# Performance work log

Hardware: AMD Instinct MI355X
Metric: run time of the kernel (lower is better)

## Reference

```python
import jax, jax.numpy as jnp
import numpy as np

EMB = 512
LIN = 64
ATT = 64
H = 8
EPS = 1e-6


def layer_norm(x, eps=EPS):
    # layer norm over last dim, no affine params (matches F.layer_norm w/o weight/bias)
    mu = jnp.mean(x, axis=-1, keepdims=True)
    var = jnp.var(x, axis=-1, keepdims=True)
    return (x - mu) * jax.lax.rsqrt(var + eps)


def setup_inputs() -> dict:
    key = jax.random.key(0)
    k1, k2, k3, k4, k5 = jax.random.split(key, 5)
    B, N = 8, 2048
    x = jax.random.normal(k1, (B, N, EMB), dtype=jnp.float32)
    rel_pos_bias = jax.random.normal(k2, (H, N, N), dtype=jnp.float32)
    invalid_attn_mask = jnp.ones((B, N, N), dtype=jnp.float32)
    uvqk = jax.random.normal(k3, (EMB, LIN * 2 * H + ATT * H * 2), dtype=jnp.float32) * 0.02
    o_w = jax.random.normal(k4, (EMB, LIN * H), dtype=jnp.float32) * (1.0 / np.sqrt(LIN * H))
    o_b = jnp.zeros((EMB,), dtype=jnp.float32)
    return {"x": x, "rel_pos_bias": rel_pos_bias, "invalid_attn_mask": invalid_attn_mask,
            "uvqk": uvqk, "o_w": o_w, "o_b": o_b}


def reference(x, rel_pos_bias, invalid_attn_mask, uvqk, o_w, o_b):
    B, N, D = x.shape
    residual = x
    normed = layer_norm(x)                                   # [B,N,D]
    proj = jax.nn.silu(jnp.einsum('bnd,de->bne', normed, uvqk))  # [B,N,2*LIN*H+2*ATT*H]
    lh = LIN * H
    ah = ATT * H
    u = proj[..., :lh]                                        # [B,N,LIN*H]
    v = proj[..., lh:2 * lh].reshape(B, N, H, LIN)            # [B,N,H,LIN]
    q = proj[..., 2 * lh:2 * lh + ah].reshape(B, N, H, ATT)
    k = proj[..., 2 * lh + ah:].reshape(B, N, H, ATT)
    qk = jnp.einsum('bnhd,bmhd->bhnm', q, k) + rel_pos_bias[None]  # [B,H,N,N]
    qk = jax.nn.silu(qk) * invalid_attn_mask[:, None]
    attn = jnp.einsum('bhnm,bmhd->bnhd', qk, v).reshape(B, N, lh)
    gated = u * layer_norm(attn)
    out = jnp.einsum('bnf,ef->bne', gated, o_w) + o_b          # dropout off (eval)
    return residual + out
```

## Files before the change

kernel.cpp:

```cpp
#include <hip/hip_runtime.h>
#include <stdint.h>

typedef short bf16x8   __attribute__((ext_vector_type(8)));
typedef short short4v  __attribute__((ext_vector_type(4)));
typedef short short8v  __attribute__((ext_vector_type(8)));
typedef float f32x4    __attribute__((ext_vector_type(4)));

typedef __attribute__((address_space(3))) uint32_t lds_u32;
typedef const __attribute__((address_space(1))) uint32_t glob_u32;

__device__ __forceinline__ void gl_lds16(const void* g, void* l) {
  __builtin_amdgcn_global_load_lds((glob_u32*)g, (lds_u32*)l, 16, 0, 0);
}

__device__ __forceinline__ float bf2f(short u) {
  union { float f; uint32_t i; } v; v.i = ((uint32_t)(uint16_t)u) << 16; return v.f;
}
__device__ __forceinline__ short f2bf(float f) {
  union { float f; uint32_t i; } v; v.f = f;
  uint32_t r = v.i + 0x7FFFu + ((v.i >> 16) & 1u);
  return (short)(r >> 16);
}
__device__ __forceinline__ float siluf(float x) {
  return x * __builtin_amdgcn_rcpf(1.0f + __expf(-x));
}
__device__ __forceinline__ f32x4 mfma16(bf16x8 a, bf16x8 b, f32x4 c) {
  return __builtin_amdgcn_mfma_f32_16x16x32_bf16(a, b, c, 0, 0, 0);
}

__global__ __launch_bounds__(256) void k_ln(const float* __restrict__ x, short* __restrict__ xn) {
  int row = blockIdx.x * 4 + (threadIdx.x >> 6);
  int lane = threadIdx.x & 63;
  const float4* xr = (const float4*)(x + (size_t)row * 512);
  float4 a = xr[lane * 2], b = xr[lane * 2 + 1];
  float s  = a.x + a.y + a.z + a.w + b.x + b.y + b.z + b.w;
  float s2 = a.x*a.x + a.y*a.y + a.z*a.z + a.w*a.w + b.x*b.x + b.y*b.y + b.z*b.z + b.w*b.w;
#pragma unroll
  for (int m = 1; m < 64; m <<= 1) { s += __shfl_xor(s, m); s2 += __shfl_xor(s2, m); }
  float mu = s * (1.f / 512.f);
  float rstd = rsqrtf(s2 * (1.f / 512.f) - mu * mu + 1e-6f);
  float v[8] = {a.x, a.y, a.z, a.w, b.x, b.y, b.z, b.w};
  short8v o;
#pragma unroll
  for (int j = 0; j < 8; ++j) o[j] = f2bf((v[j] - mu) * rstd);
  *(short8v*)&xn[(size_t)row * 512 + lane * 8] = o;
}

__global__ __launch_bounds__(256) void k_prep_w(const float* __restrict__ uvqk, short* __restrict__ Wt) {
  __shared__ float t[64][65];
  int k0 = blockIdx.x * 64;
  int c0 = blockIdx.y * 64;
  for (int i = threadIdx.x; i < 64 * 64; i += 256) {
    int r = i >> 6, c = i & 63;
    t[r][c] = uvqk[(size_t)(k0 + r) * 2048 + c0 + c];
  }
  __syncthreads();
  for (int i = threadIdx.x; i < 64 * 64; i += 256) {
    int c = i >> 6, k = i & 63;
    Wt[(size_t)(c0 + c) * 512 + k0 + k] = f2bf(t[k][c]);
  }
}

__global__ __launch_bounds__(256) void k_cast_ow(const float* __restrict__ ow, short* __restrict__ owt) {
  int i = blockIdx.x * 256 + threadIdx.x;
  owt[i] = f2bf(ow[i]);
}

__device__ __forceinline__ void gemm_core(const short* __restrict__ A, const short* __restrict__ Bt,
                                          int t0, int c0, short* As, short* Bs, f32x4 (&acc)[4][4]) {
  int tid = threadIdx.x;
  int w = tid >> 6, lane = tid & 63, l16 = lane & 15, lq = lane >> 4;
  int wm = (w >> 1) * 64, wn = (w & 1) * 64;
  int srow = tid >> 3;
  int sch = (tid & 7) ^ (srow & 7);
  const short* ag = A  + (size_t)(t0 + srow) * 512 + sch * 8;
  const short* bg = Bt + (size_t)(c0 + srow) * 512 + sch * 8;

  for (int k0 = 0; k0 < 512; k0 += 64) {
#pragma unroll
    for (int j = 0; j < 4; ++j) {
      gl_lds16(ag + (size_t)j * 32 * 512 + k0, (char*)As + j * 4096 + w * 1024);
      gl_lds16(bg + (size_t)j * 32 * 512 + k0, (char*)Bs + j * 4096 + w * 1024);
    }
    asm volatile("s_waitcnt vmcnt(0)" ::: "memory");
    __syncthreads();
#pragma unroll
    for (int kk = 0; kk < 2; ++kk) {
      bf16x8 af[4], bf[4];
#pragma unroll
      for (int mi = 0; mi < 4; ++mi) {
        int row = wm + mi * 16 + l16;
        af[mi] = *(const bf16x8*)&As[row * 64 + (((kk * 4 + lq) ^ (l16 & 7)) * 8)];
      }
#pragma unroll
      for (int ni = 0; ni < 4; ++ni) {
        int row = wn + ni * 16 + l16;
        bf[ni] = *(const bf16x8*)&Bs[row * 64 + (((kk * 4 + lq) ^ (l16 & 7)) * 8)];
      }
#pragma unroll
      for (int mi = 0; mi < 4; ++mi)
#pragma unroll
        for (int ni = 0; ni < 4; ++ni)
          acc[mi][ni] = mfma16(af[mi], bf[ni], acc[mi][ni]);
    }
    __syncthreads();
  }
}

__global__ __launch_bounds__(256) void k_gemm1(const short* __restrict__ A, const short* __restrict__ Bt,
                                               short* __restrict__ proj, short* __restrict__ Vt) {
  __shared__ short As[128 * 64], Bs[128 * 64];
  int c0 = blockIdx.x * 128, t0 = blockIdx.y * 128;
  f32x4 acc[4][4] = {};
  gemm_core(A, Bt, t0, c0, As, Bs, acc);
  int tid = threadIdx.x, w = tid >> 6, lane = tid & 63, l16 = lane & 15, lq = lane >> 4;
  int wm = (w >> 1) * 64, wn = (w & 1) * 64;
  bool isv = (c0 >= 512 && c0 < 1024);
#pragma unroll
  for (int mi = 0; mi < 4; ++mi)
#pragma unroll
    for (int ni = 0; ni < 4; ++ni) {
      int c = c0 + wn + ni * 16 + l16;
      int trow = t0 + wm + mi * 16 + lq * 4;
      if (isv) {
        int hh = (c - 512) >> 6, d = (c - 512) & 63;
        int bb = trow >> 11, nn = trow & 2047;
        short4v pv;
#pragma unroll
        for (int i = 0; i < 4; ++i) pv[i] = f2bf(siluf(acc[mi][ni][i]));
        *(short4v*)&Vt[((size_t)(bb * 8 + hh) * 64 + d) * 2048 + nn] = pv;
      } else {
#pragma unroll
        for (int i = 0; i < 4; ++i)
          proj[(size_t)(trow + i) * 2048 + c] = f2bf(siluf(acc[mi][ni][i]));
      }
    }
}

__global__ __launch_bounds__(256, 3) void k_attn(const short* __restrict__ proj,
                                                 const short* __restrict__ Vt,
                                                 const float* __restrict__ rpb,
                                                 const float* __restrict__ maskp,
                                                 float* __restrict__ attn) {
  __shared__ __align__(16) short Ks[2][64 * 64];
  __shared__ __align__(16) short Vs[2][64 * 64];
  __shared__ __align__(16) short Ps[128 * 64];

  int p = blockIdx.x;
  int L = (p & 7) * 128 + (p >> 3);
  int qt = L >> 6, h = (L >> 3) & 7, b = L & 7;
  int n0 = qt * 128;

  int tid = threadIdx.x;
  int w = tid >> 6, lane = tid & 63, l16 = lane & 15, lq = lane >> 4;

  bf16x8 qf[2][2];
#pragma unroll
  for (int mi = 0; mi < 2; ++mi)
#pragma unroll
    for (int kk = 0; kk < 2; ++kk) {
      int n = n0 + w * 32 + mi * 16 + l16;
      qf[mi][kk] = *(const bf16x8*)&proj[(size_t)(b * 2048 + n) * 2048 + 1024 + h * 64 + kk * 32 + lq * 8];
    }

  int j8 = lane >> 3, c8 = lane & 7;
  int srcc = (c8 ^ j8) * 8;
  const short* kg = proj + (size_t)(b * 2048) * 2048 + 1536 + h * 64 + srcc;
  const short* vg = Vt + (size_t)((b * 8 + h) * 64) * 2048 + srcc;

  const float* rp_t = rpb   + (size_t)h * 4194304 + (size_t)(n0 + w * 32 + l16) * 2048 + lq * 4;
  const float* mk_t = maskp + (size_t)b * 4194304 + (size_t)(n0 + w * 32 + l16) * 2048 + lq * 4;

  f32x4 acc_o[2][4] = {};

#pragma unroll
  for (int j = 0; j < 2; ++j) {
    gl_lds16(kg + (size_t)(w * 16 + j * 8 + j8) * 2048, &Ks[0][w * 1024 + j * 512]);
    gl_lds16(vg + (size_t)(w * 16 + j * 8 + j8) * 2048, &Vs[0][w * 1024 + j * 512]);
  }
  asm volatile("s_waitcnt vmcnt(0)" ::: "memory");
  __builtin_amdgcn_s_barrier();

  for (int t = 0; t < 32; ++t) {
    int kv0 = t << 6;
    const short* Kc = Ks[t & 1];
    const short* Vc = Vs[t & 1];

    if (t < 31) {
      short* Kn = Ks[(t & 1) ^ 1];
      short* Vn = Vs[(t & 1) ^ 1];
      int kvn = kv0 + 64;
#pragma unroll
      for (int j = 0; j < 2; ++j) {
        gl_lds16(kg + (size_t)(kvn + w * 16 + j * 8 + j8) * 2048, &Kn[w * 1024 + j * 512]);
        gl_lds16(vg + (size_t)(w * 16 + j * 8 + j8) * 2048 + kvn, &Vn[w * 1024 + j * 512]);
      }
    }

    f32x4 rv0[4], mv0[4];
#pragma unroll
    for (int ni = 0; ni < 4; ++ni) {
      rv0[ni] = *(const f32x4*)(rp_t + kv0 + ni * 16);
      mv0[ni] = *(const f32x4*)(mk_t + kv0 + ni * 16);
    }

    f32x4 s[4][2];
#pragma unroll
    for (int ni = 0; ni < 4; ++ni)
#pragma unroll
      for (int mi = 0; mi < 2; ++mi) s[ni][mi] = (f32x4){0.f, 0.f, 0.f, 0.f};
    __builtin_amdgcn_s_setprio(1);
#pragma unroll
    for (int kk = 0; kk < 2; ++kk) {
      bf16x8 kf[4];
#pragma unroll
      for (int ni = 0; ni < 4; ++ni)
        kf[ni] = *(const bf16x8*)&Kc[(ni * 16 + l16) * 64 + (((kk * 4 + lq) ^ (l16 & 7)) * 8)];
#pragma unroll
      for (int ni = 0; ni < 4; ++ni)
#pragma unroll
        for (int mi = 0; mi < 2; ++mi)
          s[ni][mi] = mfma16(kf[ni], qf[mi][kk], s[ni][mi]);
    }
    __builtin_amdgcn_s_setprio(0);

    f32x4 rv1[4], mv1[4];
#pragma unroll
    for (int ni = 0; ni < 4; ++ni) {
      rv1[ni] = *(const f32x4*)(rp_t + 16 * 2048 + kv0 + ni * 16);
      mv1[ni] = *(const f32x4*)(mk_t + 16 * 2048 + kv0 + ni * 16);
    }

    {
      int row = w * 32 + l16;
      char* pr = (char*)Ps + row * 128;
      int swz = (l16 & 7) << 4;
#pragma unroll
      for (int ni = 0; ni < 4; ++ni) {
        short4v pk;
#pragma unroll
        for (int i = 0; i < 4; ++i) {
          float xx = s[ni][0][i] + rv0[ni][i];
          pk[i] = f2bf(siluf(xx) * mv0[ni][i]);
        }
        *(short4v*)(pr + ((ni * 32 + lq * 8) ^ swz)) = pk;
      }
    }
    {
      int row = w * 32 + 16 + l16;
      char* pr = (char*)Ps + row * 128;
      int swz = (l16 & 7) << 4;
#pragma unroll
      for (int ni = 0; ni < 4; ++ni) {
        short4v pk;
#pragma unroll
        for (int i = 0; i < 4; ++i) {
          float xx = s[ni][1][i] + rv1[ni][i];
          pk[i] = f2bf(siluf(xx) * mv1[ni][i]);
        }
        *(short4v*)(pr + ((ni * 32 + lq * 8) ^ swz)) = pk;
      }
    }

    __builtin_amdgcn_s_setprio(1);
#pragma unroll
    for (int ks = 0; ks < 2; ++ks) {
      bf16x8 pf[2], vf[4];
#pragma unroll
      for (int mi = 0; mi < 2; ++mi) {
        int rp = w * 32 + mi * 16 + l16;
        pf[mi] = *(const bf16x8*)((const char*)Ps + rp * 128 + (((ks * 4 + lq) << 4) ^ ((l16 & 7) << 4)));
      }
#pragma unroll
      for (int ni = 0; ni < 4; ++ni)
        vf[ni] = *(const bf16x8*)&Vc[(ni * 16 + l16) * 64 + (((ks * 4 + lq) ^ (l16 & 7)) * 8)];
#pragma unroll
      for (int mi = 0; mi < 2; ++mi)
#pragma unroll
        for (int ni = 0; ni < 4; ++ni)
          acc_o[mi][ni] = mfma16(pf[mi], vf[ni], acc_o[mi][ni]);
    }
    __builtin_amdgcn_s_setprio(0);

    asm volatile("s_waitcnt vmcnt(0)" ::: "memory");
    __builtin_amdgcn_s_barrier();
  }

#pragma unroll
  for (int mi = 0; mi < 2; ++mi)
#pragma unroll
    for (int ni = 0; ni < 4; ++ni)
#pragma unroll
      for (int i = 0; i < 4; ++i) {
        int n = n0 + w * 32 + mi * 16 + lq * 4 + i;
        attn[(size_t)(b * 2048 + n) * 512 + h * 64 + ni * 16 + l16] = acc_o[mi][ni][i];
      }
}

__global__ __launch_bounds__(256) void k_gate(const float* __restrict__ attn, const short* __restrict__ proj,
                                              short* __restrict__ gated) {
  int row = blockIdx.x * 4 + (threadIdx.x >> 6);
  int lane = threadIdx.x & 63;
  const float4* ar = (const float4*)(attn + (size_t)row * 512);
  float4 a = ar[lane * 2], b = ar[lane * 2 + 1];
  float s  = a.x + a.y + a.z + a.w + b.x + b.y + b.z + b.w;
  float s2 = a.x*a.x + a.y*a.y + a.z*a.z + a.w*a.w + b.x*b.x + b.y*b.y + b.z*b.z + b.w*b.w;
#pragma unroll
  for (int m = 1; m < 64; m <<= 1) { s += __shfl_xor(s, m); s2 += __shfl_xor(s2, m); }
  float mu = s * (1.f / 512.f);
  float rstd = rsqrtf(s2 * (1.f / 512.f) - mu * mu + 1e-6f);
  float v[8] = {a.x, a.y, a.z, a.w, b.x, b.y, b.z, b.w};
  short8v u = *(const short8v*)&proj[(size_t)row * 2048 + lane * 8];
  short8v g;
#pragma unroll
  for (int j = 0; j < 8; ++j) g[j] = f2bf(bf2f(u[j]) * ((v[j] - mu) * rstd));
  *(short8v*)&gated[(size_t)row * 512 + lane * 8] = g;
}

__global__ __launch_bounds__(256) void k_gemm2(const short* __restrict__ A, const short* __restrict__ Bt,
                                               const float* __restrict__ ob, const float* __restrict__ x,
                                               float* __restrict__ out) {
  __shared__ short As[128 * 64], Bs[128 * 64];
  int c0 = blockIdx.x * 128, t0 = blockIdx.y * 128;
  f32x4 acc[4][4] = {};
  gemm_core(A, Bt, t0, c0, As, Bs, acc);
  int tid = threadIdx.x, w = tid >> 6, lane = tid & 63, l16 = lane & 15, lq = lane >> 4;
  int wm = (w >> 1) * 64, wn = (w & 1) * 64;
#pragma unroll
  for (int mi = 0; mi < 4; ++mi)
#pragma unroll
    for (int ni = 0; ni < 4; ++ni) {
      int e = c0 + wn + ni * 16 + l16;
      float bias = ob[e];
#pragma unroll
      for (int i = 0; i < 4; ++i) {
        int t = t0 + wm + mi * 16 + lq * 4 + i;
        out[(size_t)t * 512 + e] = acc[mi][ni][i] + bias + x[(size_t)t * 512 + e];
      }
    }
}

extern "C" void kernel_launch(void* const* d_in, const int* in_sizes, int n_in,
                              void* d_out, int out_size, void* d_ws, size_t ws_size,
                              hipStream_t stream) {
  const float* x    = (const float*)d_in[0];
  const float* rpb  = (const float*)d_in[1];
  const float* mask = (const float*)d_in[2];
  const float* uvqk = (const float*)d_in[3];
  const float* o_w  = (const float*)d_in[4];
  const float* o_b  = (const float*)d_in[5];
  float* out = (float*)d_out;

  char* p = (char*)d_ws;
  short* xn   = (short*)p; p += 16384ull * 512 * 2;
  short* Wt   = (short*)p; p += 2048ull * 512 * 2;
  short* owt  = (short*)p; p += 512ull * 512 * 2;
  short* proj = (short*)p; p += 16384ull * 2048 * 2;
  short* Vt   = (short*)p; p += 8ull * 8 * 64 * 2048 * 2;
  float* attn = (float*)p; p += 16384ull * 512 * 4;
  short* gated = xn;

  k_ln    <<<4096, 256, 0, stream>>>(x, xn);
  k_prep_w<<<dim3(8, 32), 256, 0, stream>>>(uvqk, Wt);
  k_cast_ow<<<1024, 256, 0, stream>>>(o_w, owt);
  k_gemm1 <<<dim3(16, 128), 256, 0, stream>>>(xn, Wt, proj, Vt);
  k_attn  <<<1024, 256, 0, stream>>>(proj, Vt, rpb, mask, attn);
  k_gate  <<<4096, 256, 0, stream>>>(attn, proj, gated);
  k_gemm2 <<<dim3(4, 128), 256, 0, stream>>>(gated, owt, o_b, x, out);
}
```

Before: 392.3 us.

## Cast bias and mask to bf16 and prefetch them one tile ahead

Adds a vectorised cast kernel that converts the relative position bias and the attention mask to bf16 in workspace on every call. The attention kernel is templated so it reads these half-width copies when the workspace is large enough. It also loads the bias and mask values for the next KV tile at the end of each iteration, waiting with a partial vmcnt instead of a full drain. This roughly halves the bias and mask traffic that each attention block re-reads across heads and batches, at the price of an extra full pass over both fp32 tensors and bf16 rounding of the bias.

```diff
diff --git a/kernel.cpp b/kernel.cpp
--- a/kernel.cpp
+++ b/kernel.cpp
@@ -64,6 +64,18 @@
 __global__ __launch_bounds__(256) void k_cast_ow(const float* __restrict__ ow, short* __restrict__ owt) {
   int i = blockIdx.x * 256 + threadIdx.x;
   owt[i] = f2bf(ow[i]);
+}
+
+__global__ __launch_bounds__(256) void k_cast_bf(const float* __restrict__ src, short* __restrict__ dst, int n8) {
+  for (int i = blockIdx.x * 256 + threadIdx.x; i < n8; i += gridDim.x * 256) {
+    const float4* s4 = (const float4*)src + (size_t)i * 2;
+    float4 a = s4[0], b = s4[1];
+    float v[8] = {a.x, a.y, a.z, a.w, b.x, b.y, b.z, b.w};
+    short8v o;
+#pragma unroll
+    for (int j = 0; j < 8; ++j) o[j] = f2bf(v[j]);
+    *(short8v*)&dst[(size_t)i * 8] = o;
+  }
 }
 
 __device__ __forceinline__ void gemm_core(const short* __restrict__ A, const short* __restrict__ Bt,
@@ -137,10 +149,11 @@
     }
 }
 
+template<bool BF>
 __global__ __launch_bounds__(256, 3) void k_attn(const short* __restrict__ proj,
                                                  const short* __restrict__ Vt,
-                                                 const float* __restrict__ rpb,
-                                                 const float* __restrict__ maskp,
+                                                 const void* __restrict__ rpbp,
+                                                 const void* __restrict__ maskp,
                                                  float* __restrict__ attn) {
   __shared__ __align__(16) short Ks[2][64 * 64];
   __shared__ __align__(16) short Vs[2][64 * 64];
@@ -168,17 +181,36 @@
   const short* kg = proj + (size_t)(b * 2048) * 2048 + 1536 + h * 64 + srcc;
   const short* vg = Vt + (size_t)((b * 8 + h) * 64) * 2048 + srcc;
 
-  const float* rp_t = rpb   + (size_t)h * 4194304 + (size_t)(n0 + w * 32 + l16) * 2048 + lq * 4;
-  const float* mk_t = maskp + (size_t)b * 4194304 + (size_t)(n0 + w * 32 + l16) * 2048 + lq * 4;
+  size_t rbase = (size_t)h * 4194304 + (size_t)(n0 + w * 32 + l16) * 2048 + lq * 4;
+  size_t mbase = (size_t)b * 4194304 + (size_t)(n0 + w * 32 + l16) * 2048 + lq * 4;
 
   f32x4 acc_o[2][4] = {};
+
+  short4v rvb[2][4], mvb[2][4];
+  f32x4   rvf[2][4], mvf[2][4];
 
 #pragma unroll
   for (int j = 0; j < 2; ++j) {
     gl_lds16(kg + (size_t)(w * 16 + j * 8 + j8) * 2048, &Ks[0][w * 1024 + j * 512]);
     gl_lds16(vg + (size_t)(w * 16 + j * 8 + j8) * 2048, &Vs[0][w * 1024 + j * 512]);
   }
-  asm volatile("s_waitcnt vmcnt(0)" ::: "memory");
+  __builtin_amdgcn_sched_barrier(0);
+#pragma unroll
+  for (int mi = 0; mi < 2; ++mi)
+#pragma unroll
+    for (int ni = 0; ni < 4; ++ni) {
+      size_t off = (size_t)mi * 16 * 2048 + ni * 16;
+      if constexpr (BF) {
+        rvb[mi][ni] = *(const short4v*)((const short*)rpbp + rbase + off);
+        mvb[mi][ni] = *(const short4v*)((const short*)maskp + mbase + off);
+      } else {
+        rvf[mi][ni] = *(const f32x4*)((const float*)rpbp + rbase + off);
+        mvf[mi][ni] = *(const f32x4*)((const float*)maskp + mbase + off);
+      }
+    }
+  __builtin_amdgcn_sched_barrier(0);
+  asm volatile("s_waitcnt vmcnt(16)" ::: "memory");
+  __builtin_amdgcn_sched_barrier(0);
   __builtin_amdgcn_s_barrier();
 
   for (int t = 0; t < 32; ++t) {
@@ -196,13 +228,7 @@
         gl_lds16(vg + (size_t)(w * 16 + j * 8 + j8) * 2048 + kvn, &Vn[w * 1024 + j * 512]);
       }
     }
-
-    f32x4 rv0[4], mv0[4];
-#pragma unroll
-    for (int ni = 0; ni < 4; ++ni) {
-      rv0[ni] = *(const f32x4*)(rp_t + kv0 + ni * 16);
-      mv0[ni] = *(const f32x4*)(mk_t + kv0 + ni * 16);
-    }
+    __builtin_amdgcn_sched_barrier(0);
 
     f32x4 s[4][2];
 #pragma unroll
@@ -224,15 +250,9 @@
     }
     __builtin_amdgcn_s_setprio(0);
 
-    f32x4 rv1[4], mv1[4];
-#pragma unroll
-    for (int ni = 0; ni < 4; ++ni) {
-      rv1[ni] = *(const f32x4*)(rp_t + 16 * 2048 + kv0 + ni * 16);
-      mv1[ni] = *(const f32x4*)(mk_t + 16 * 2048 + kv0 + ni * 16);
-    }
-
-    {
-      int row = w * 32 + l16;
+#pragma unroll
+    for (int mi = 0; mi < 2; ++mi) {
+      int row = w * 32 + mi * 16 + l16;
       char* pr = (char*)Ps + row * 128;
       int swz = (l16 & 7) << 4;
 #pragma unroll
@@ -240,23 +260,11 @@
         short4v pk;
 #pragma unroll
         for (int i = 0; i < 4; ++i) {
-          float xx = s[ni][0][i] + rv0[ni][i];
-          pk[i] = f2bf(siluf(xx) * mv0[ni][i]);
-        }
-        *(short4v*)(pr + ((ni * 32 + lq * 8) ^ swz)) = pk;
-      }
-    }
-    {
-      int row = w * 32 + 16 + l16;
-      char* pr = (char*)Ps + row * 128;
-      int swz = (l16 & 7) << 4;
-#pragma unroll
-      for (int ni = 0; ni < 4; ++ni) {
-        short4v pk;
-#pragma unroll
-        for (int i = 0; i < 4; ++i) {
-          float xx = s[ni][1][i] + rv1[ni][i];
-          pk[i] = f2bf(siluf(xx) * mv1[ni][i]);
+          float r, m;
+          if constexpr (BF) { r = bf2f(rvb[mi][ni][i]); m = bf2f(mvb[mi][ni][i]); }
+          else              { r = rvf[mi][ni][i];       m = mvf[mi][ni][i]; }
+          float xx = s[ni][mi][i] + r;
+          pk[i] = f2bf(siluf(xx) * m);
         }
         *(short4v*)(pr + ((ni * 32 + lq * 8) ^ swz)) = pk;
       }
@@ -282,7 +290,26 @@
     }
     __builtin_amdgcn_s_setprio(0);
 
-    asm volatile("s_waitcnt vmcnt(0)" ::: "memory");
+    __builtin_amdgcn_sched_barrier(0);
+    {
+      int kvp = (t < 31) ? kv0 + 64 : kv0;
+#pragma unroll
+      for (int mi = 0; mi < 2; ++mi)
+#pragma unroll
+        for (int ni = 0; ni < 4; ++ni) {
+          size_t off = (size_t)mi * 16 * 2048 + kvp + ni * 16;
+          if constexpr (BF) {
+            rvb[mi][ni] = *(const short4v*)((const short*)rpbp + rbase + off);
+            mvb[mi][ni] = *(const short4v*)((const short*)maskp + mbase + off);
+          } else {
+            rvf[mi][ni] = *(const f32x4*)((const float*)rpbp + rbase + off);
+            mvf[mi][ni] = *(const f32x4*)((const float*)maskp + mbase + off);
+          }
+        }
+    }
+    __builtin_amdgcn_sched_barrier(0);
+    asm volatile("s_waitcnt vmcnt(16)" ::: "memory");
+    __builtin_amdgcn_sched_barrier(0);
     __builtin_amdgcn_s_barrier();
   }
 
@@ -358,13 +385,24 @@
   short* proj = (short*)p; p += 16384ull * 2048 * 2;
   short* Vt   = (short*)p; p += 8ull * 8 * 64 * 2048 * 2;
   float* attn = (float*)p; p += 16384ull * 512 * 4;
+  short* rpbh = (short*)p; p += 33554432ull * 2;
+  short* mskh = (short*)p; p += 33554432ull * 2;
   short* gated = xn;
+
+  bool bf_ok = ws_size >= (size_t)((char*)p - (char*)d_ws);
 
   k_ln    <<<4096, 256, 0, stream>>>(x, xn);
   k_prep_w<<<dim3(8, 32), 256, 0, stream>>>(uvqk, Wt);
   k_cast_ow<<<1024, 256, 0, stream>>>(o_w, owt);
+  if (bf_ok) {
+    k_cast_bf<<<4096, 256, 0, stream>>>(rpb,  rpbh, 33554432 / 8);
+    k_cast_bf<<<4096, 256, 0, stream>>>(mask, mskh, 33554432 / 8);
+  }
   k_gemm1 <<<dim3(16, 128), 256, 0, stream>>>(xn, Wt, proj, Vt);
-  k_attn  <<<1024, 256, 0, stream>>>(proj, Vt, rpb, mask, attn);
+  if (bf_ok)
+    k_attn<true> <<<1024, 256, 0, stream>>>(proj, Vt, rpbh, mskh, attn);
+  else
+    k_attn<false><<<1024, 256, 0, stream>>>(proj, Vt, rpb, mask, attn);
   k_gate  <<<4096, 256, 0, stream>>>(attn, proj, gated);
   k_gemm2 <<<dim3(4, 128), 256, 0, stream>>>(gated, owt, o_b, x, out);
 }
```

Measured after the change: 477.6 us. 21.8% more time.

## Halve attention query tile, prefetch bias/mask one step ahead, use packed bf16 convert

Applied to the files above, without the earlier changes.

The attention kernel now handles 64 query rows per block instead of 128 and launches twice as many blocks. It also declares 4 waves per SIMD in launch bounds instead of 3 and halves the P scratch buffer. The rel_pos_bias and mask loads for the next KV tile are issued at the end of each iteration, with a partial vmcnt wait, so the dominant fp32 bias and mask streams overlap compute. The P tile is converted with v_cvt_pk_bf16_f32 instead of manual rounding. Smaller tiles double K/V reloads from L2 in exchange for higher occupancy and latency hiding.

```diff
diff --git a/kernel.cpp b/kernel.cpp
--- a/kernel.cpp
+++ b/kernel.cpp
@@ -26,6 +26,11 @@
 }
 __device__ __forceinline__ f32x4 mfma16(bf16x8 a, bf16x8 b, f32x4 c) {
   return __builtin_amdgcn_mfma_f32_16x16x32_bf16(a, b, c, 0, 0, 0);
+}
+__device__ __forceinline__ uint32_t cvtpk_bf16(float lo, float hi) {
+  uint32_t d;
+  asm("v_cvt_pk_bf16_f32 %0, %1, %2" : "=v"(d) : "v"(lo), "v"(hi));
+  return d;
 }
 
 __global__ __launch_bounds__(256) void k_ln(const float* __restrict__ x, short* __restrict__ xn) {
@@ -137,48 +142,55 @@
     }
 }
 
-__global__ __launch_bounds__(256, 3) void k_attn(const short* __restrict__ proj,
+__global__ __launch_bounds__(256, 4) void k_attn(const short* __restrict__ proj,
                                                  const short* __restrict__ Vt,
                                                  const float* __restrict__ rpb,
                                                  const float* __restrict__ maskp,
                                                  float* __restrict__ attn) {
   __shared__ __align__(16) short Ks[2][64 * 64];
   __shared__ __align__(16) short Vs[2][64 * 64];
-  __shared__ __align__(16) short Ps[128 * 64];
+  __shared__ __align__(16) short Ps[64 * 64];
 
   int p = blockIdx.x;
-  int L = (p & 7) * 128 + (p >> 3);
+  int L = (p & 7) * 256 + (p >> 3);
   int qt = L >> 6, h = (L >> 3) & 7, b = L & 7;
-  int n0 = qt * 128;
+  int n0 = qt * 64;
 
   int tid = threadIdx.x;
   int w = tid >> 6, lane = tid & 63, l16 = lane & 15, lq = lane >> 4;
 
-  bf16x8 qf[2][2];
-#pragma unroll
-  for (int mi = 0; mi < 2; ++mi)
-#pragma unroll
-    for (int kk = 0; kk < 2; ++kk) {
-      int n = n0 + w * 32 + mi * 16 + l16;
-      qf[mi][kk] = *(const bf16x8*)&proj[(size_t)(b * 2048 + n) * 2048 + 1024 + h * 64 + kk * 32 + lq * 8];
-    }
+  bf16x8 qf[2];
+#pragma unroll
+  for (int kk = 0; kk < 2; ++kk) {
+    int n = n0 + w * 16 + l16;
+    qf[kk] = *(const bf16x8*)&proj[(size_t)(b * 2048 + n) * 2048 + 1024 + h * 64 + kk * 32 + lq * 8];
+  }
 
   int j8 = lane >> 3, c8 = lane & 7;
   int srcc = (c8 ^ j8) * 8;
   const short* kg = proj + (size_t)(b * 2048) * 2048 + 1536 + h * 64 + srcc;
   const short* vg = Vt + (size_t)((b * 8 + h) * 64) * 2048 + srcc;
 
-  const float* rp_t = rpb   + (size_t)h * 4194304 + (size_t)(n0 + w * 32 + l16) * 2048 + lq * 4;
-  const float* mk_t = maskp + (size_t)b * 4194304 + (size_t)(n0 + w * 32 + l16) * 2048 + lq * 4;
-
-  f32x4 acc_o[2][4] = {};
+  const float* rp_t = rpb   + (size_t)h * 4194304 + (size_t)(n0 + w * 16 + l16) * 2048 + lq * 4;
+  const float* mk_t = maskp + (size_t)b * 4194304 + (size_t)(n0 + w * 16 + l16) * 2048 + lq * 4;
+
+  f32x4 acc_o[4] = {};
+  f32x4 rv[4], mv[4];
 
 #pragma unroll
   for (int j = 0; j < 2; ++j) {
     gl_lds16(kg + (size_t)(w * 16 + j * 8 + j8) * 2048, &Ks[0][w * 1024 + j * 512]);
     gl_lds16(vg + (size_t)(w * 16 + j * 8 + j8) * 2048, &Vs[0][w * 1024 + j * 512]);
   }
-  asm volatile("s_waitcnt vmcnt(0)" ::: "memory");
+  __builtin_amdgcn_sched_barrier(0);
+#pragma unroll
+  for (int ni = 0; ni < 4; ++ni) {
+    rv[ni] = *(const f32x4*)(rp_t + ni * 16);
+    mv[ni] = *(const f32x4*)(mk_t + ni * 16);
+  }
+  __builtin_amdgcn_sched_barrier(0);
+  asm volatile("s_waitcnt vmcnt(8)" ::: "memory");
+  __builtin_amdgcn_sched_barrier(0);
   __builtin_amdgcn_s_barrier();
 
   for (int t = 0; t < 32; ++t) {
@@ -196,19 +208,11 @@
         gl_lds16(vg + (size_t)(w * 16 + j * 8 + j8) * 2048 + kvn, &Vn[w * 1024 + j * 512]);
       }
     }
-
-    f32x4 rv0[4], mv0[4];
-#pragma unroll
-    for (int ni = 0; ni < 4; ++ni) {
-      rv0[ni] = *(const f32x4*)(rp_t + kv0 + ni * 16);
-      mv0[ni] = *(const f32x4*)(mk_t + kv0 + ni * 16);
-    }
-
-    f32x4 s[4][2];
-#pragma unroll
-    for (int ni = 0; ni < 4; ++ni)
-#pragma unroll
-      for (int mi = 0; mi < 2; ++mi) s[ni][mi] = (f32x4){0.f, 0.f, 0.f, 0.f};
+    __builtin_amdgcn_sched_barrier(0);
+
+    f32x4 s[4];
+#pragma unroll
+    for (int ni = 0; ni < 4; ++ni) s[ni] = (f32x4){0.f, 0.f, 0.f, 0.f};
     __builtin_amdgcn_s_setprio(1);
 #pragma unroll
     for (int kk = 0; kk < 2; ++kk) {
@@ -218,83 +222,68 @@
         kf[ni] = *(const bf16x8*)&Kc[(ni * 16 + l16) * 64 + (((kk * 4 + lq) ^ (l16 & 7)) * 8)];
 #pragma unroll
       for (int ni = 0; ni < 4; ++ni)
-#pragma unroll
-        for (int mi = 0; mi < 2; ++mi)
-          s[ni][mi] = mfma16(kf[ni], qf[mi][kk], s[ni][mi]);
+        s[ni] = mfma16(kf[ni], qf[kk], s[ni]);
     }
     __builtin_amdgcn_s_setprio(0);
 
-    f32x4 rv1[4], mv1[4];
-#pragma unroll
-    for (int ni = 0; ni < 4; ++ni) {
-      rv1[ni] = *(const f32x4*)(rp_t + 16 * 2048 + kv0 + ni * 16);
-      mv1[ni] = *(const f32x4*)(mk_t + 16 * 2048 + kv0 + ni * 16);
-    }
-
     {
-      int row = w * 32 + l16;
+      int row = w * 16 + l16;
       char* pr = (char*)Ps + row * 128;
       int swz = (l16 & 7) << 4;
 #pragma unroll
       for (int ni = 0; ni < 4; ++ni) {
-        short4v pk;
+        float pv[4];
 #pragma unroll
         for (int i = 0; i < 4; ++i) {
-          float xx = s[ni][0][i] + rv0[ni][i];
-          pk[i] = f2bf(siluf(xx) * mv0[ni][i]);
+          float xx = s[ni][i] + rv[ni][i];
+          pv[i] = siluf(xx) * mv[ni][i];
         }
-        *(short4v*)(pr + ((ni * 32 + lq * 8) ^ swz)) = pk;
-      }
-    }
-    {
-      int row = w * 32 + 16 + l16;
-      char* pr = (char*)Ps + row * 128;
-      int swz = (l16 & 7) << 4;
-#pragma unroll
-      for (int ni = 0; ni < 4; ++ni) {
-        short4v pk;
-#pragma unroll
-        for (int i = 0; i < 4; ++i) {
-          float xx = s[ni][1][i] + rv1[ni][i];
-          pk[i] = f2bf(siluf(xx) * mv1[ni][i]);
-        }
-        *(short4v*)(pr + ((ni * 32 + lq * 8) ^ swz)) = pk;
+        union { uint32_t u[2]; short4v sv; } pk;
+        pk.u[0] = cvtpk_bf16(pv[0], pv[1]);
+        pk.u[1] = cvtpk_bf16(pv[2], pv[3]);
+        *(short4v*)(pr + ((ni * 32 + lq * 8) ^ swz)) = pk.sv;
       }
     }
 
     __builtin_amdgcn_s_setprio(1);
 #pragma unroll
     for (int ks = 0; ks < 2; ++ks) {
-      bf16x8 pf[2], vf[4];
-#pragma unroll
-      for (int mi = 0; mi < 2; ++mi) {
-        int rp = w * 32 + mi * 16 + l16;
-        pf[mi] = *(const bf16x8*)((const char*)Ps + rp * 128 + (((ks * 4 + lq) << 4) ^ ((l16 & 7) << 4)));
+      bf16x8 pf, vf[4];
+      {
+        int rp = w * 16 + l16;
+        pf = *(const bf16x8*)((const char*)Ps + rp * 128 + (((ks * 4 + lq) << 4) ^ ((l16 & 7) << 4)));
       }
 #pragma unroll
       for (int ni = 0; ni < 4; ++ni)
         vf[ni] = *(const bf16x8*)&Vc[(ni * 16 + l16) * 64 + (((ks * 4 + lq) ^ (l16 & 7)) * 8)];
 #pragma unroll
-      for (int mi = 0; mi < 2; ++mi)
-#pragma unroll
-        for (int ni = 0; ni < 4; ++ni)
-          acc_o[mi][ni] = mfma16(pf[mi], vf[ni], acc_o[mi][ni]);
+      for (int ni = 0; ni < 4; ++ni)
+        acc_o[ni] = mfma16(pf, vf[ni], acc_o[ni]);
     }
     __builtin_amdgcn_s_setprio(0);
 
-    asm volatile("s_waitcnt vmcnt(0)" ::: "memory");
+    __builtin_amdgcn_sched_barrier(0);
+    {
+      int kvp = (t < 31) ? kv0 + 64 : kv0;
+#pragma unroll
+      for (int ni = 0; ni < 4; ++ni) {
+        rv[ni] = *(const f32x4*)(rp_t + kvp + ni * 16);
+        mv[ni] = *(const f32x4*)(mk_t + kvp + ni * 16);
+      }
+    }
+    __builtin_amdgcn_sched_barrier(0);
+    asm volatile("s_waitcnt vmcnt(8)" ::: "memory");
+    __builtin_amdgcn_sched_barrier(0);
     __builtin_amdgcn_s_barrier();
   }
 
 #pragma unroll
-  for (int mi = 0; mi < 2; ++mi)
-#pragma unroll
-    for (int ni = 0; ni < 4; ++ni)
-#pragma unroll
-      for (int i = 0; i < 4; ++i) {
-        int n = n0 + w * 32 + mi * 16 + lq * 4 + i;
-        attn[(size_t)(b * 2048 + n) * 512 + h * 64 + ni * 16 + l16] = acc_o[mi][ni][i];
-      }
+  for (int ni = 0; ni < 4; ++ni)
+#pragma unroll
+    for (int i = 0; i < 4; ++i) {
+      int n = n0 + w * 16 + lq * 4 + i;
+      attn[(size_t)(b * 2048 + n) * 512 + h * 64 + ni * 16 + l16] = acc_o[ni][i];
+    }
 }
 
 __global__ __launch_bounds__(256) void k_gate(const float* __restrict__ attn, const short* __restrict__ proj,
@@ -364,7 +353,7 @@
   k_prep_w<<<dim3(8, 32), 256, 0, stream>>>(uvqk, Wt);
   k_cast_ow<<<1024, 256, 0, stream>>>(o_w, owt);
   k_gemm1 <<<dim3(16, 128), 256, 0, stream>>>(xn, Wt, proj, Vt);
-  k_attn  <<<1024, 256, 0, stream>>>(proj, Vt, rpb, mask, attn);
+  k_attn  <<<2048, 256, 0, stream>>>(proj, Vt, rpb, mask, attn);
   k_gate  <<<4096, 256, 0, stream>>>(attn, proj, gated);
   k_gemm2 <<<dim3(4, 128), 256, 0, stream>>>(gated, owt, o_b, x, out);
 }
```

New measurement: 412.8 us. 1.05x slower.
